# Optimization experiments

Measured on AMD Instinct MI355X. Metric: run time of the kernel, lower is better.

## Reference

```python
import jax, jax.numpy as jnp
import numpy as np

P, S, IMG = 8, 4, 256          # patch_size, stride, img_size
HID, GH, B = 64, 128, 4        # conv hidden ch, gcn hidden ch, batch
Ph = (IMG - P) // S + 1        # 63 patches per side
N = Ph * Ph                    # 3969 patch-nodes


def _conv(x, w, b):
    y = jax.lax.conv_general_dilated(x, w, (1, 1), 'SAME',
                                     dimension_numbers=('NCHW', 'OIHW', 'NCHW'))
    return y + b[None, :, None, None]


def _img2patch(x):
    # x: [B,1,H,W] -> [B, N, P*P] (row-major patch pixels, matching torch reshape)
    pt = jax.lax.conv_general_dilated_patches(x, (P, P), (S, S), 'VALID')  # [B, P*P, Ph, Pw]
    b = x.shape[0]
    return pt.reshape(b, P * P, N).transpose(0, 2, 1)


def _patch2img(y):
    # y: [b, N, P*P] -> [b, 1, IMG, IMG] via overlap scatter-add
    b = y.shape[0]
    y = y.reshape(b, Ph, Ph, P, P)
    x = jnp.zeros((b, 1, IMG, IMG), y.dtype)
    hi = S * (Ph - 1) + 1
    for i in range(P):          # fixed small loop over patch pixels (64 iters)
        for j in range(P):
            x = x.at[:, 0, i:i + hi:S, j:j + hi:S].add(y[:, :, :, i, j])
    return x


def _gcn(x, adj, w, bias):
    # x: [B,N,F_in], adj: [B,N,N] -> [B,N,F_out]
    support = jnp.einsum('bnf,fg->bng', x, w)
    return jnp.einsum('bnm,bmg->bng', adj, support) + bias


def setup_inputs() -> dict:
    key = jax.random.key(0)
    ks = jax.random.split(key, 14)
    sc = 0.05
    return {
        'input_data': jax.random.normal(ks[0], (B, 1, IMG, IMG), jnp.float32),
        'proj': jax.random.normal(ks[1], (B, 1, IMG, IMG), jnp.float32),
        'adj': jax.random.uniform(ks[2], (B, N, N), jnp.float32) / N,
        'lam': jnp.float32(0.5),
        'conv_w1': jax.random.normal(ks[3], (HID, 1, 3, 3), jnp.float32) * sc,
        'conv_b1': jnp.zeros((HID,), jnp.float32),
        'conv_w2': jax.random.normal(ks[4], (HID, HID, 3, 3), jnp.float32) * sc,
        'conv_b2': jnp.zeros((HID,), jnp.float32),
        'conv_w3': jax.random.normal(ks[5], (1, HID, 3, 3), jnp.float32) * sc,
        'conv_b3': jnp.zeros((1,), jnp.float32),
        'gcn_w3': jax.random.normal(ks[6], (P * P, GH), jnp.float32) * sc,
        'gcn_b3': jnp.zeros((GH,), jnp.float32),
        'gcn_w4': jax.random.normal(ks[7], (GH, P * P), jnp.float32) * sc,
        'gcn_b4': jnp.zeros((P * P,), jnp.float32),
    }


def reference(input_data, proj, adj, lam,
              conv_w1, conv_b1, conv_w2, conv_b2, conv_w3, conv_b3,
              gcn_w3, gcn_b3, gcn_w4, gcn_b4):
    # block1: data-fidelity step (fidelity_module modeled as DC update)
    tmp1 = input_data + lam * (proj - input_data)
    # block2: 3-layer CNN
    h = jax.nn.relu(_conv(input_data, conv_w1, conv_b1))
    h = jax.nn.relu(_conv(h, conv_w2, conv_b2))
    tmp2 = _conv(h, conv_w3, conv_b3)
    # block3/4: patch-graph GCN branch
    patch = _img2patch(input_data)                 # [B, N, P*P]
    g = jax.nn.relu(_gcn(patch, adj, gcn_w3, gcn_b3))
    g = _gcn(g, adj, gcn_w4, gcn_b4)               # [B, N, P*P]
    # Patch2Im with overlap-count normalization mask
    mask = _patch2img(jnp.ones((1, N, P * P), jnp.float32))
    tmp3 = _patch2img(g) / mask
    return jax.nn.relu(tmp1 + tmp2 + tmp3)
```

## Files before the change

### kernel.cpp

```cpp
#include <hip/hip_runtime.h>

#define IMG   256
#define NPIX  65536
#define PH    63
#define NNODE 3969
#define SN    4000
#define SN2   4096
#define HID   64
#define GH    128
#define BATCH 4

typedef __attribute__((ext_vector_type(8))) short short8;
typedef __attribute__((ext_vector_type(4))) float float4v;
typedef unsigned short ushort_t;

__device__ inline ushort_t f2bf(float f) {
    union { float f; unsigned u; } v; v.f = f;
    unsigned r = v.u + 0x7FFF + ((v.u >> 16) & 1);
    return (ushort_t)(r >> 16);
}
__device__ inline unsigned pk2(float a, float b) {
    return (unsigned)f2bf(a) | ((unsigned)f2bf(b) << 16);
}

__global__ __launch_bounds__(256) void k_cvt_adj(const float* __restrict__ adj,
                                                 ushort_t* __restrict__ adjb) {
    int n = blockIdx.x, b = blockIdx.y;
    const float* src = adj + (size_t)(b * NNODE + n) * NNODE;
    unsigned* dst = (unsigned*)(adjb + (size_t)(b * NNODE + n) * SN);
    for (int c2 = threadIdx.x; c2 < SN / 2; c2 += 256) {
        int c = c2 * 2;
        float f0 = (c < NNODE) ? src[c] : 0.f;
        float f1 = (c + 1 < NNODE) ? src[c + 1] : 0.f;
        dst[c2] = pk2(f0, f1);
    }
}

__global__ __launch_bounds__(256) void k_prepack(const float* __restrict__ cw2,
                                                 const float* __restrict__ w3,
                                                 const float* __restrict__ w4,
                                                 ushort_t* __restrict__ W2p,
                                                 ushort_t* __restrict__ w3p,
                                                 ushort_t* __restrict__ w4p) {
    int idx = blockIdx.x * 256 + threadIdx.x;
    if (idx < 36864) {
        int tap = idx >> 12, rem = idx & 4095;
        int oc = rem >> 6, ic = rem & 63;
        W2p[idx] = f2bf(cw2[(oc * 64 + ic) * 9 + tap]);
    } else if (idx < 45056) {
        int i2 = idx - 36864;
        int g = i2 >> 6, pix = i2 & 63;
        w3p[i2] = f2bf(w3[pix * GH + g]);
    } else if (idx < 53248) {
        int i3 = idx - 45056;
        int g = i3 >> 7, k = i3 & 127;
        w4p[i3] = f2bf(w4[k * 64 + g]);
    }
}

__global__ __launch_bounds__(256) void k_sup1(const float* __restrict__ in,
                                              const ushort_t* __restrict__ w3p,
                                              ushort_t* __restrict__ sup1T) {
    __shared__ ushort_t Ps[128][72];
    const int b = blockIdx.z;
    const int n0 = blockIdx.x * 128;
    const float* inb = in + (size_t)b * NPIX;
    const int t = threadIdx.x;
    const int lane = t & 63, w = t >> 6;
    const int l15 = lane & 15, q = lane >> 4;

    for (int idx = t; idx < 1024; idx += 256) {
        int nl = idx >> 3, i = idx & 7;
        int n = n0 + nl;
        unsigned pk[4] = {0u, 0u, 0u, 0u};
        if (n < NNODE) {
            int py = n / PH, px = n - py * PH;
            const float* rp = inb + (py * 4 + i) * IMG + px * 4;
            float4 a = *(const float4*)rp;
            float4 c = *(const float4*)(rp + 4);
            pk[0] = pk2(a.x, a.y); pk[1] = pk2(a.z, a.w);
            pk[2] = pk2(c.x, c.y); pk[3] = pk2(c.z, c.w);
        }
        *(uint4*)&Ps[nl][i * 8] = *(uint4*)pk;
    }
    __syncthreads();

    const int g0 = (w & 1) * 64, nw = (w >> 1) * 64;
    float4v acc[4][4];
#pragma unroll
    for (int i = 0; i < 4; ++i)
#pragma unroll
        for (int j = 0; j < 4; ++j)
#pragma unroll
            for (int r = 0; r < 4; ++r) acc[i][j][r] = 0.f;

#pragma unroll
    for (int c = 0; c < 2; ++c) {
        short8 af[4], bf[4];
#pragma unroll
        for (int i = 0; i < 4; ++i)
            af[i] = *(const short8*)&w3p[(g0 + i * 16 + l15) * 64 + c * 32 + q * 8];
#pragma unroll
        for (int j = 0; j < 4; ++j)
            bf[j] = *(const short8*)&Ps[nw + j * 16 + l15][c * 32 + q * 8];
#pragma unroll
        for (int i = 0; i < 4; ++i)
#pragma unroll
            for (int j = 0; j < 4; ++j)
                acc[i][j] = __builtin_amdgcn_mfma_f32_16x16x32_bf16(
                    af[i], bf[j], acc[i][j], 0, 0, 0);
    }
    ushort_t* dst = sup1T + (size_t)b * GH * SN;
#pragma unroll
    for (int i = 0; i < 4; ++i)
#pragma unroll
        for (int j = 0; j < 4; ++j) {
            int n = n0 + nw + j * 16 + l15;
            if (n < SN) {
                int g = g0 + i * 16 + q * 4;
#pragma unroll
                for (int r = 0; r < 4; ++r)
                    dst[(size_t)(g + r) * SN + n] = f2bf(acc[i][j][r]);
            }
        }
}

template <int G, bool TRANS>
__global__ __launch_bounds__(256) void k_gemm_mfma(const ushort_t* __restrict__ adjb,
                                                   const ushort_t* __restrict__ supT,
                                                   float* __restrict__ C) {
    constexpr int FN = (G == 128) ? 4 : 2;
    const int b = blockIdx.z, ks = blockIdx.y;
    const int node0 = blockIdx.x * 128;
    const int t = threadIdx.x;
    const int lane = t & 63, w = t >> 6;
    const int l15 = lane & 15, q = lane >> 4;
    const int wm0 = (G == 128) ? (w & 1) * 64 : 0;
    const int wn0 = (G == 128) ? (w >> 1) * 64 : w * 32;

    __shared__ ushort_t Als[G][40];
    __shared__ ushort_t Bls[128][40];

    const int k0c = ks * 992;
    const int kend = (ks == 3) ? NNODE : k0c + 992;
    const int kiters = (kend - k0c + 31) >> 5;

    const ushort_t* Ab = supT + (size_t)b * G * SN;
    const ushort_t* Bb = adjb + (size_t)b * NNODE * SN;

    float4v acc[4][FN];
#pragma unroll
    for (int i = 0; i < 4; ++i)
#pragma unroll
        for (int j = 0; j < FN; ++j)
#pragma unroll
            for (int r = 0; r < 4; ++r) acc[i][j][r] = 0.f;

    for (int kk = 0; kk < kiters; ++kk) {
        const int kbase = k0c + kk * 32;
#pragma unroll
        for (int i = 0; i < G / 64; ++i) {
            int idx = t + i * 256;
            int r = idx >> 2, s = idx & 3;
            *(uint4*)&Als[r][s * 8] =
                *(const uint4*)&Ab[(size_t)r * SN + kbase + s * 8];
        }
#pragma unroll
        for (int i = 0; i < 2; ++i) {
            int idx = t + i * 256;
            int r = idx >> 2, s = idx & 3;
            *(uint4*)&Bls[r][s * 8] =
                *(const uint4*)&Bb[(size_t)(node0 + r) * SN + kbase + s * 8];
        }
        __syncthreads();
        short8 af[4], bf[FN];
#pragma unroll
        for (int i = 0; i < 4; ++i)
            af[i] = *(const short8*)&Als[wm0 + i * 16 + l15][q * 8];
#pragma unroll
        for (int j = 0; j < FN; ++j)
            bf[j] = *(const short8*)&Bls[wn0 + j * 16 + l15][q * 8];
#pragma unroll
        for (int i = 0; i < 4; ++i)
#pragma unroll
            for (int j = 0; j < FN; ++j)
                acc[i][j] = __builtin_amdgcn_mfma_f32_16x16x32_bf16(
                    af[i], bf[j], acc[i][j], 0, 0, 0);
        __syncthreads();
    }
    if (TRANS) {
        float* Cb = C + (size_t)b * SN2 * 128;
#pragma unroll
        for (int i = 0; i < 4; ++i) {
            int gg = wm0 + i * 16 + q * 4;
#pragma unroll
            for (int j = 0; j < FN; ++j) {
                int nn = node0 + wn0 + j * 16 + l15;
                if (nn < NNODE) {
#pragma unroll
                    for (int r = 0; r < 4; ++r)
                        unsafeAtomicAdd(&Cb[(size_t)nn * 128 + gg + r], acc[i][j][r]);
                }
            }
        }
    } else {
        float* Cb = C + (size_t)b * G * SN;
#pragma unroll
        for (int i = 0; i < 4; ++i) {
            int gg = wm0 + i * 16 + q * 4;
#pragma unroll
            for (int j = 0; j < FN; ++j) {
                int nn = node0 + wn0 + j * 16 + l15;
                if (nn < NNODE) {
#pragma unroll
                    for (int r = 0; r < 4; ++r)
                        unsafeAtomicAdd(&Cb[(size_t)(gg + r) * SN + nn], acc[i][j][r]);
                }
            }
        }
    }
}

__global__ __launch_bounds__(256) void k_act(const float* __restrict__ g1n,
                                             const float* __restrict__ gb3,
                                             ushort_t* __restrict__ a1t) {
    int idx = blockIdx.x * 256 + threadIdx.x;
    int b = idx >> 16, rem = idx & 65535;
    int n = rem >> 4, kg = rem & 15;
    const float* src = g1n + ((size_t)b * SN2 + n) * 128 + kg * 8;
    float4 a = *(const float4*)src;
    float4 c = *(const float4*)(src + 4);
    float4 ba = *(const float4*)(gb3 + kg * 8);
    float4 bc = *(const float4*)(gb3 + kg * 8 + 4);
    unsigned pk[4];
    pk[0] = pk2(fmaxf(a.x + ba.x, 0.f), fmaxf(a.y + ba.y, 0.f));
    pk[1] = pk2(fmaxf(a.z + ba.z, 0.f), fmaxf(a.w + ba.w, 0.f));
    pk[2] = pk2(fmaxf(c.x + bc.x, 0.f), fmaxf(c.y + bc.y, 0.f));
    pk[3] = pk2(fmaxf(c.z + bc.z, 0.f), fmaxf(c.w + bc.w, 0.f));
    *(uint4*)(a1t + ((size_t)b * SN2 + n) * 128 + kg * 8) = *(uint4*)pk;
}

__global__ __launch_bounds__(256) void k_gemm_s2(const ushort_t* __restrict__ a1t,
                                                 const ushort_t* __restrict__ w4p,
                                                 ushort_t* __restrict__ sup2T) {
    __shared__ ushort_t Ls[128][136];
    const int b = blockIdx.y;
    const int n0 = blockIdx.x * 128;
    const int t = threadIdx.x;
    const int lane = t & 63, w = t >> 6;
    const int l15 = lane & 15, q = lane >> 4;

    const ushort_t* src = a1t + (size_t)b * SN2 * 128;
    for (int idx = t; idx < 2048; idx += 256) {
        int nl = idx >> 4, kg = idx & 15;
        *(uint4*)&Ls[nl][kg * 8] =
            *(const uint4*)&src[(size_t)(n0 + nl) * 128 + kg * 8];
    }
    __syncthreads();

    const int nw = w * 32;
    float4v acc[4][2];
#pragma unroll
    for (int i = 0; i < 4; ++i)
#pragma unroll
        for (int j = 0; j < 2; ++j)
#pragma unroll
            for (int r = 0; r < 4; ++r) acc[i][j][r] = 0.f;

#pragma unroll
    for (int c = 0; c < 4; ++c) {
        short8 af[4], bf[2];
#pragma unroll
        for (int i = 0; i < 4; ++i)
            af[i] = *(const short8*)&w4p[(i * 16 + l15) * 128 + c * 32 + q * 8];
#pragma unroll
        for (int j = 0; j < 2; ++j)
            bf[j] = *(const short8*)&Ls[nw + j * 16 + l15][c * 32 + q * 8];
#pragma unroll
        for (int i = 0; i < 4; ++i)
#pragma unroll
            for (int j = 0; j < 2; ++j)
                acc[i][j] = __builtin_amdgcn_mfma_f32_16x16x32_bf16(
                    af[i], bf[j], acc[i][j], 0, 0, 0);
    }
    ushort_t* dst = sup2T + (size_t)b * 64 * SN;
#pragma unroll
    for (int i = 0; i < 4; ++i)
#pragma unroll
        for (int j = 0; j < 2; ++j) {
            int n = n0 + nw + j * 16 + l15;
            if (n < SN) {
                int g = i * 16 + q * 4;
#pragma unroll
                for (int r = 0; r < 4; ++r)
                    dst[(size_t)(g + r) * SN + n] = f2bf(acc[i][j][r]);
            }
        }
}

__global__ __launch_bounds__(256) void k_conv1(const float* __restrict__ in,
                                               const float* __restrict__ w,
                                               const float* __restrict__ bias,
                                               ushort_t* __restrict__ h1n) {
    int b = blockIdx.z;
    const float* inb = in + (size_t)b * NPIX;
    __shared__ float s[18][18];
    __shared__ float ws[576];
    int tx = threadIdx.x & 15, ty = threadIdx.x >> 4;
    int x0 = blockIdx.x * 16, y0 = blockIdx.y * 16;
    for (int idx = threadIdx.x; idx < 324; idx += 256) {
        int yy = idx / 18, xx = idx - yy * 18;
        int gy = y0 + yy - 1, gx = x0 + xx - 1;
        s[yy][xx] = (gy >= 0 && gy < IMG && gx >= 0 && gx < IMG) ? inb[gy * IMG + gx] : 0.f;
    }
    for (int idx = threadIdx.x; idx < 576; idx += 256) ws[idx] = w[idx];
    __syncthreads();
    float r[9];
#pragma unroll
    for (int dy = 0; dy < 3; ++dy)
#pragma unroll
        for (int dx = 0; dx < 3; ++dx) r[dy * 3 + dx] = s[ty + dy][tx + dx];
    int outp = (y0 + ty) * IMG + x0 + tx;
    ushort_t* dst = h1n + ((size_t)b * NPIX + outp) * 64;
#pragma unroll
    for (int sgrp = 0; sgrp < 8; ++sgrp) {
        unsigned pk[4];
#pragma unroll
        for (int h = 0; h < 4; ++h) {
            int oc0 = sgrp * 8 + h * 2;
            float a0 = bias[oc0], a1 = bias[oc0 + 1];
#pragma unroll
            for (int k = 0; k < 9; ++k) {
                a0 += r[k] * ws[oc0 * 9 + k];
                a1 += r[k] * ws[(oc0 + 1) * 9 + k];
            }
            pk[h] = pk2(fmaxf(a0, 0.f), fmaxf(a1, 0.f));
        }
        *(uint4*)&dst[sgrp * 8] = *(uint4*)pk;
    }
}

__global__ __launch_bounds__(256) void k_conv2(const ushort_t* __restrict__ h1n,
                                               const ushort_t* __restrict__ W2p,
                                               const float* __restrict__ bias,
                                               float* __restrict__ h2) {
    __shared__ ushort_t Xs[340 * 72];
    const int b = blockIdx.z;
    const ushort_t* h1b = h1n + (size_t)b * NPIX * 64;
    float* h2b = h2 + (size_t)b * 64 * NPIX;
    const int t = threadIdx.x;
    const int lane = t & 63, w = t >> 6;
    const int l15 = lane & 15, q = lane >> 4;
    const int x0 = blockIdx.x * 32, y0 = blockIdx.y * 8;

    for (int idx = t; idx < 2720; idx += 256) {
        int hp = idx >> 3, s = idx & 7;
        int hy = hp / 34, hx = hp - hy * 34;
        int gy = y0 + hy - 1, gx = x0 + hx - 1;
        uint4 v = {0u, 0u, 0u, 0u};
        if (gy >= 0 && gy < IMG && gx >= 0 && gx < IMG)
            v = *(const uint4*)&h1b[((size_t)gy * IMG + gx) * 64 + s * 8];
        *(uint4*)&Xs[hp * 72 + s * 8] = v;
    }
    __syncthreads();

    const int wn0 = w * 64;
    int pbase[4];
#pragma unroll
    for (int j = 0; j < 4; ++j) {
        int p = wn0 + j * 16 + l15;
        pbase[j] = (p >> 5) * 34 + (p & 31);
    }

    float4v acc[4][4];
#pragma unroll
    for (int i = 0; i < 4; ++i)
#pragma unroll
        for (int j = 0; j < 4; ++j)
#pragma unroll
            for (int r = 0; r < 4; ++r) acc[i][j][r] = 0.f;

    for (int tap = 0; tap < 9; ++tap) {
        int ky = tap / 3, kx = tap - ky * 3;
        const ushort_t* wp = W2p + tap * 4096;
#pragma unroll
        for (int c = 0; c < 2; ++c) {
            short8 af[4], bf[4];
#pragma unroll
            for (int i = 0; i < 4; ++i)
                af[i] = *(const short8*)&wp[(i * 16 + l15) * 64 + c * 32 + q * 8];
#pragma unroll
            for (int j = 0; j < 4; ++j)
                bf[j] = *(const short8*)&Xs[(pbase[j] + ky * 34 + kx) * 72 + c * 32 + q * 8];
#pragma unroll
            for (int i = 0; i < 4; ++i)
#pragma unroll
                for (int j = 0; j < 4; ++j)
                    acc[i][j] = __builtin_amdgcn_mfma_f32_16x16x32_bf16(
                        af[i], bf[j], acc[i][j], 0, 0, 0);
        }
    }
#pragma unroll
    for (int i = 0; i < 4; ++i) {
#pragma unroll
        for (int j = 0; j < 4; ++j) {
            int p = wn0 + j * 16 + l15;
            int y = y0 + (p >> 5), x = x0 + (p & 31);
#pragma unroll
            for (int r = 0; r < 4; ++r) {
                int oc = i * 16 + q * 4 + r;
                h2b[(size_t)oc * NPIX + (size_t)y * IMG + x] =
                    fmaxf(acc[i][j][r] + bias[oc], 0.f);
            }
        }
    }
}

__global__ __launch_bounds__(256) void k_combine(const float* __restrict__ in,
                                                 const float* __restrict__ proj,
                                                 const float* __restrict__ lamp,
                                                 const float* __restrict__ h2,
                                                 const float* __restrict__ wc,
                                                 const float* __restrict__ bc,
                                                 const float* __restrict__ g2T,
                                                 const float* __restrict__ gb4,
                                                 float* __restrict__ out) {
    int b = blockIdx.z;
    const float* inb = in + (size_t)b * NPIX;
    const float* prb = proj + (size_t)b * NPIX;
    const float* h2b = h2 + (size_t)b * 64 * NPIX;
    const float* g2b = g2T + (size_t)b * 64 * SN;
    __shared__ float s[16][18][18];
    __shared__ float ws[144];
    int tx = threadIdx.x & 15, ty = threadIdx.x >> 4;
    int x0 = blockIdx.x * 16, y0 = blockIdx.y * 16;
    int y = y0 + ty, x = x0 + tx;

    float acc = bc[0];
    for (int icc = 0; icc < 4; ++icc) {
        for (int idx = threadIdx.x; idx < 16 * 324; idx += 256) {
            int ic = idx / 324, rem = idx - ic * 324;
            int yy = rem / 18, xx = rem - yy * 18;
            int gy = y0 + yy - 1, gx = x0 + xx - 1;
            s[ic][yy][xx] = (gy >= 0 && gy < IMG && gx >= 0 && gx < IMG)
                                ? h2b[(icc * 16 + ic) * NPIX + gy * IMG + gx]
                                : 0.f;
        }
        for (int idx = threadIdx.x; idx < 144; idx += 256) ws[idx] = wc[icc * 144 + idx];
        __syncthreads();
#pragma unroll 4
        for (int ic = 0; ic < 16; ++ic) {
#pragma unroll
            for (int ky = 0; ky < 3; ++ky)
#pragma unroll
                for (int kx = 0; kx < 3; ++kx)
                    acc += s[ic][ty + ky][tx + kx] * ws[ic * 9 + ky * 3 + kx];
        }
        __syncthreads();
    }

    float iv = inb[y * IMG + x], pv = prb[y * IMG + x];
    float tmp1 = iv + lamp[0] * (pv - iv);

    int pylo = (y >= 4) ? ((y - 4) >> 2) : 0;
    int pyhi = min(62, y >> 2);
    int pxlo = (x >= 4) ? ((x - 4) >> 2) : 0;
    int pxhi = min(62, x >> 2);
    float sum = 0.f;
    int cnt = 0;
    for (int py = pylo; py <= pyhi; ++py)
        for (int px = pxlo; px <= pxhi; ++px) {
            int pix = (y - 4 * py) * 8 + (x - 4 * px);
            sum += g2b[(size_t)pix * SN + (py * PH + px)] + gb4[pix];
            ++cnt;
        }
    float tmp3 = sum / (float)cnt;

    out[(size_t)b * NPIX + y * IMG + x] = fmaxf(tmp1 + acc + tmp3, 0.f);
}

extern "C" void kernel_launch(void* const* d_in, const int* in_sizes, int n_in,
                              void* d_out, int out_size, void* d_ws, size_t ws_size,
                              hipStream_t stream) {
    const float* input = (const float*)d_in[0];
    const float* proj  = (const float*)d_in[1];
    const float* adj   = (const float*)d_in[2];
    const float* lam   = (const float*)d_in[3];
    const float* cw1   = (const float*)d_in[4];
    const float* cb1   = (const float*)d_in[5];
    const float* cw2   = (const float*)d_in[6];
    const float* cb2   = (const float*)d_in[7];
    const float* cw3   = (const float*)d_in[8];
    const float* cb3   = (const float*)d_in[9];
    const float* gw3   = (const float*)d_in[10];
    const float* gb3   = (const float*)d_in[11];
    const float* gw4   = (const float*)d_in[12];
    const float* gb4   = (const float*)d_in[13];
    float* out = (float*)d_out;

    char* base = (char*)d_ws;
    float*    g2T   = (float*)(base);
    ushort_t* adjb  = (ushort_t*)(base + 4096000);
    ushort_t* sup1T = (ushort_t*)(base + 131104000);
    float*    g1n   = (float*)(base + 135200000);
    ushort_t* a1t   = (ushort_t*)(base + 143588608);
    ushort_t* sup2T = (ushort_t*)(base + 147782912);
    ushort_t* w3p   = (ushort_t*)(base + 149830912);
    ushort_t* w4p   = (ushort_t*)(base + 149847296);
    ushort_t* W2p   = (ushort_t*)(base + 149863680);
    ushort_t* h1n   = (ushort_t*)(base + 149937408);
    float*    h2    = (float*)(base + 183491840);

    dim3 blk(256);

    hipMemsetAsync(g1n, 0, (size_t)BATCH * SN2 * 128 * 4, stream);
    hipMemsetAsync(g2T, 0, (size_t)BATCH * 64 * SN * 4, stream);

    k_prepack<<<dim3(208), blk, 0, stream>>>(cw2, gw3, gw4, W2p, w3p, w4p);
    k_cvt_adj<<<dim3(NNODE, BATCH), blk, 0, stream>>>(adj, adjb);

    k_sup1<<<dim3(32, 1, BATCH), blk, 0, stream>>>(input, w3p, sup1T);
    k_gemm_mfma<128, true><<<dim3(32, 4, BATCH), blk, 0, stream>>>(adjb, sup1T, g1n);
    k_act<<<dim3(1024), blk, 0, stream>>>(g1n, gb3, a1t);
    k_gemm_s2<<<dim3(32, BATCH), blk, 0, stream>>>(a1t, w4p, sup2T);
    k_gemm_mfma<64, false><<<dim3(32, 4, BATCH), blk, 0, stream>>>(adjb, sup2T, g2T);

    k_conv1<<<dim3(16, 16, BATCH), blk, 0, stream>>>(input, cw1, cb1, h1n);
    k_conv2<<<dim3(8, 32, BATCH), blk, 0, stream>>>(h1n, W2p, cb2, h2);
    k_combine<<<dim3(16, 16, BATCH), blk, 0, stream>>>(
        input, proj, lam, h2, cw3, cb3, g2T, gb4, out);
}
```

Measured before the change: 719.7 us.

## Load MFMA operands directly from global memory, dropping LDS staging in GCN GEMMs

The adjacency GEMM kernel no longer stages A and B tiles through shared memory with two barriers per 32-wide K step. Each wave now loads its own bf16 fragments straight from global memory with per-row pointers, using a 2x unrolled loop. To support this, the node stride is padded to 4032 and the K split is realigned to 1024-element chunks. The small support GEMM also drops its LDS staging in the same way. This removes barrier and LDS traffic, at the cost of duplicated global and L2 reads across waves and 64-byte strided access per row.

```diff
diff --git a/kernel.cpp b/kernel.cpp
--- a/kernel.cpp
+++ b/kernel.cpp
@@ -4,7 +4,7 @@
 #define NPIX  65536
 #define PH    63
 #define NNODE 3969
-#define SN    4000
+#define SN    4032
 #define SN2   4096
 #define HID   64
 #define GH    128
@@ -132,21 +132,25 @@
     constexpr int FN = (G == 128) ? 4 : 2;
     const int b = blockIdx.z, ks = blockIdx.y;
     const int node0 = blockIdx.x * 128;
-    const int t = threadIdx.x;
-    const int lane = t & 63, w = t >> 6;
+    const int lane = threadIdx.x & 63, w = threadIdx.x >> 6;
     const int l15 = lane & 15, q = lane >> 4;
     const int wm0 = (G == 128) ? (w & 1) * 64 : 0;
     const int wn0 = (G == 128) ? (w >> 1) * 64 : w * 32;
 
-    __shared__ ushort_t Als[G][40];
-    __shared__ ushort_t Bls[128][40];
-
-    const int k0c = ks * 992;
-    const int kend = (ks == 3) ? NNODE : k0c + 992;
-    const int kiters = (kend - k0c + 31) >> 5;
-
-    const ushort_t* Ab = supT + (size_t)b * G * SN;
-    const ushort_t* Bb = adjb + (size_t)b * NNODE * SN;
+    const int kb0 = ks * 1024;
+    const int citers = (ks == 3) ? 30 : 32;
+
+    const ushort_t* Ab = supT + (size_t)b * G * SN + kb0 + q * 8;
+    const ushort_t* Bb = adjb + (size_t)b * NNODE * SN + kb0 + q * 8;
+
+    const ushort_t* Ap[4];
+#pragma unroll
+    for (int i = 0; i < 4; ++i)
+        Ap[i] = Ab + (size_t)(wm0 + i * 16 + l15) * SN;
+    const ushort_t* Bp[FN];
+#pragma unroll
+    for (int j = 0; j < FN; ++j)
+        Bp[j] = Bb + (size_t)(node0 + wn0 + j * 16 + l15) * SN;
 
     float4v acc[4][FN];
 #pragma unroll
@@ -156,38 +160,21 @@
 #pragma unroll
             for (int r = 0; r < 4; ++r) acc[i][j][r] = 0.f;
 
-    for (int kk = 0; kk < kiters; ++kk) {
-        const int kbase = k0c + kk * 32;
-#pragma unroll
-        for (int i = 0; i < G / 64; ++i) {
-            int idx = t + i * 256;
-            int r = idx >> 2, s = idx & 3;
-            *(uint4*)&Als[r][s * 8] =
-                *(const uint4*)&Ab[(size_t)r * SN + kbase + s * 8];
-        }
-#pragma unroll
-        for (int i = 0; i < 2; ++i) {
-            int idx = t + i * 256;
-            int r = idx >> 2, s = idx & 3;
-            *(uint4*)&Bls[r][s * 8] =
-                *(const uint4*)&Bb[(size_t)(node0 + r) * SN + kbase + s * 8];
-        }
-        __syncthreads();
+#pragma unroll 2
+    for (int c = 0; c < citers; ++c) {
         short8 af[4], bf[FN];
 #pragma unroll
-        for (int i = 0; i < 4; ++i)
-            af[i] = *(const short8*)&Als[wm0 + i * 16 + l15][q * 8];
-#pragma unroll
-        for (int j = 0; j < FN; ++j)
-            bf[j] = *(const short8*)&Bls[wn0 + j * 16 + l15][q * 8];
+        for (int i = 0; i < 4; ++i) af[i] = *(const short8*)(Ap[i] + c * 32);
+#pragma unroll
+        for (int j = 0; j < FN; ++j) bf[j] = *(const short8*)(Bp[j] + c * 32);
 #pragma unroll
         for (int i = 0; i < 4; ++i)
 #pragma unroll
             for (int j = 0; j < FN; ++j)
                 acc[i][j] = __builtin_amdgcn_mfma_f32_16x16x32_bf16(
                     af[i], bf[j], acc[i][j], 0, 0, 0);
-        __syncthreads();
-    }
+    }
+
     if (TRANS) {
         float* Cb = C + (size_t)b * SN2 * 128;
 #pragma unroll
@@ -243,22 +230,18 @@
 __global__ __launch_bounds__(256) void k_gemm_s2(const ushort_t* __restrict__ a1t,
                                                  const ushort_t* __restrict__ w4p,
                                                  ushort_t* __restrict__ sup2T) {
-    __shared__ ushort_t Ls[128][136];
     const int b = blockIdx.y;
     const int n0 = blockIdx.x * 128;
-    const int t = threadIdx.x;
-    const int lane = t & 63, w = t >> 6;
+    const int lane = threadIdx.x & 63, w = threadIdx.x >> 6;
     const int l15 = lane & 15, q = lane >> 4;
-
-    const ushort_t* src = a1t + (size_t)b * SN2 * 128;
-    for (int idx = t; idx < 2048; idx += 256) {
-        int nl = idx >> 4, kg = idx & 15;
-        *(uint4*)&Ls[nl][kg * 8] =
-            *(const uint4*)&src[(size_t)(n0 + nl) * 128 + kg * 8];
-    }
-    __syncthreads();
-
     const int nw = w * 32;
+
+    const ushort_t* src = a1t + (size_t)b * SN2 * 128 + q * 8;
+    const ushort_t* Bp[2];
+#pragma unroll
+    for (int j = 0; j < 2; ++j)
+        Bp[j] = src + (size_t)(n0 + nw + j * 16 + l15) * 128;
+
     float4v acc[4][2];
 #pragma unroll
     for (int i = 0; i < 4; ++i)
@@ -275,7 +258,7 @@
             af[i] = *(const short8*)&w4p[(i * 16 + l15) * 128 + c * 32 + q * 8];
 #pragma unroll
         for (int j = 0; j < 2; ++j)
-            bf[j] = *(const short8*)&Ls[nw + j * 16 + l15][c * 32 + q * 8];
+            bf[j] = *(const short8*)(Bp[j] + c * 32);
 #pragma unroll
         for (int i = 0; i < 4; ++i)
 #pragma unroll
@@ -500,16 +483,16 @@
 
     char* base = (char*)d_ws;
     float*    g2T   = (float*)(base);
-    ushort_t* adjb  = (ushort_t*)(base + 4096000);
-    ushort_t* sup1T = (ushort_t*)(base + 131104000);
-    float*    g1n   = (float*)(base + 135200000);
-    ushort_t* a1t   = (ushort_t*)(base + 143588608);
-    ushort_t* sup2T = (ushort_t*)(base + 147782912);
-    ushort_t* w3p   = (ushort_t*)(base + 149830912);
-    ushort_t* w4p   = (ushort_t*)(base + 149847296);
-    ushort_t* W2p   = (ushort_t*)(base + 149863680);
-    ushort_t* h1n   = (ushort_t*)(base + 149937408);
-    float*    h2    = (float*)(base + 183491840);
+    ushort_t* adjb  = (ushort_t*)(base + 4194304);
+    ushort_t* sup1T = (ushort_t*)(base + 134217728);
+    float*    g1n   = (float*)(base + 138412032);
+    ushort_t* a1t   = (ushort_t*)(base + 146800640);
+    ushort_t* sup2T = (ushort_t*)(base + 150994944);
+    ushort_t* w3p   = (ushort_t*)(base + 153092096);
+    ushort_t* w4p   = (ushort_t*)(base + 153108480);
+    ushort_t* W2p   = (ushort_t*)(base + 153124864);
+    ushort_t* h1n   = (ushort_t*)(base + 153198592);
+    float*    h2    = (float*)(base + 186753024);
 
     dim3 blk(256);
 
```

New measurement: 754.8 us. 1.05x slower.
